# Performance work log

Measured on AMD Instinct MI355X. Metric: run time of the kernel, lower is better.

## Reference

```python
import jax, jax.numpy as jnp
import numpy as np

B, T, C = 2, 2048, 1024
H, DK, OUT = 16, 64, 1024


def setup_inputs() -> dict:
    key = jax.random.key(0)
    k1, k2, k3, k4, k5 = jax.random.split(key, 5)
    glorot_qkv = (2.0 / (C + H * DK)) ** 0.5  # glorot_normal stddev for [C,H,DK]
    glorot_o = (2.0 / (H * DK + OUT)) ** 0.5
    return {
        "x": jax.random.normal(k1, (B, T, C), dtype=jnp.float32),
        "query_mat": jax.random.normal(k2, (C, H, DK), dtype=jnp.float32) * glorot_qkv,
        "key_mat": jax.random.normal(k3, (C, H, DK), dtype=jnp.float32) * glorot_qkv,
        "value_mat": jax.random.normal(k4, (C, H, DK), dtype=jnp.float32) * glorot_qkv,
        "linear_m1": jax.random.normal(k5, (H * DK, OUT), dtype=jnp.float32) * glorot_o,
    }


def reference(x, query_mat, key_mat, value_mat, linear_m1):
    # x: [B,T,C]; projections: [C,H,DK]
    q = jnp.einsum('btc,chd->bhtd', x, query_mat)
    k = jnp.einsum('btc,chd->bhtd', x, key_mat)
    v = jnp.einsum('btc,chd->bhtd', x, value_mat)
    d_k = query_mat.shape[-1]
    # NOTE: faithful to source, which MULTIPLIES by sqrt(d_k)
    w = jnp.einsum('bhtd,bhzd->bhtz', q, k) * (d_k ** 0.5)
    t = w.shape[-1]
    causal = jnp.tril(jnp.ones((t, t), dtype=bool))  # [T,T]
    w = jnp.where(causal, w, -jnp.inf)
    w = jax.nn.softmax(w, axis=-1)
    # dropout inactive (training=False)
    o = jnp.einsum('bhtz,bhzd->bhtd', w, v)
    o = o.transpose(0, 2, 1, 3).reshape(o.shape[0], o.shape[2], -1)  # [B,T,H*DK]
    return jnp.einsum('btc,cz->btz', o, linear_m1)
```

## Files before the change

### kernel.cpp

```cpp
#include <hip/hip_runtime.h>


typedef unsigned short u16;
typedef unsigned int u32;
typedef unsigned long long u64;
typedef __attribute__((ext_vector_type(8))) short bf16x8;
typedef __attribute__((ext_vector_type(4))) float f32x4;

__device__ inline u16 f2bf(float f) {
  union { float f; unsigned u; } v; v.f = f;
  unsigned r = v.u + 0x7FFFu + ((v.u >> 16) & 1u);
  return (u16)(r >> 16);
}
__device__ inline float bf2f(u16 h) {
  union { unsigned u; float f; } v; v.u = ((unsigned)h) << 16;
  return v.f;
}
__device__ inline void glds16(const u16* g, u16* s) {
  __builtin_amdgcn_global_load_lds(
      (const __attribute__((address_space(1))) u32*)g,
      (__attribute__((address_space(3))) u32*)s, 16, 0, 0);
}
#define MFMA __builtin_amdgcn_mfma_f32_16x16x32_bf16

__global__ __launch_bounds__(256) void split_cast(const float* __restrict__ src,
                                                  u16* __restrict__ hi,
                                                  u16* __restrict__ lo, int n) {
  int i = (blockIdx.x * 256 + threadIdx.x) * 4;
  if (i >= n) return;
  float4 v = *(const float4*)(src + i);
  ushort4 h, l;
  h.x = f2bf(v.x); l.x = f2bf(v.x - bf2f(h.x));
  h.y = f2bf(v.y); l.y = f2bf(v.y - bf2f(h.y));
  h.z = f2bf(v.z); l.z = f2bf(v.z - bf2f(h.z));
  h.w = f2bf(v.w); l.w = f2bf(v.w - bf2f(h.w));
  *(ushort4*)(hi + i) = h;
  *(ushort4*)(lo + i) = l;
}

__global__ __launch_bounds__(256) void transpose_cast(const float* __restrict__ W,
                                                      u16* __restrict__ Wt) {
  __shared__ float tile[32][33];
  int bx = blockIdx.x * 32, by = blockIdx.y * 32;
  int tx = threadIdx.x, ty = threadIdx.y;
#pragma unroll
  for (int j = 0; j < 32; j += 8)
    tile[ty + j][tx] = W[(size_t)(by + ty + j) * 1024 + bx + tx];
  __syncthreads();
#pragma unroll
  for (int j = 0; j < 32; j += 8)
    Wt[(size_t)(bx + ty + j) * 1024 + by + tx] = f2bf(tile[tx][ty + j]);
}

__global__ __launch_bounds__(256) void transpose_cast_split(const float* __restrict__ W,
                                                            u16* __restrict__ Wth,
                                                            u16* __restrict__ Wtl) {
  __shared__ float tile[32][33];
  int bx = blockIdx.x * 32, by = blockIdx.y * 32;
  int tx = threadIdx.x, ty = threadIdx.y;
#pragma unroll
  for (int j = 0; j < 32; j += 8)
    tile[ty + j][tx] = W[(size_t)(by + ty + j) * 1024 + bx + tx];
  __syncthreads();
#pragma unroll
  for (int j = 0; j < 32; j += 8) {
    float v = tile[tx][ty + j];
    u16 h = f2bf(v);
    size_t idx = (size_t)(bx + ty + j) * 1024 + by + tx;
    Wth[idx] = h;
    Wtl[idx] = f2bf(v - bf2f(h));
  }
}

__global__ __launch_bounds__(256) void gemm_qkv(
    const u16* __restrict__ Xh, const u16* __restrict__ Xl,
    const u16* __restrict__ Wqh, const u16* __restrict__ Wql,
    const u16* __restrict__ Wkh, const u16* __restrict__ Wkl,
    const u16* __restrict__ Wvt,
    u16* __restrict__ Qh, u16* __restrict__ Ql,
    u16* __restrict__ Kh, u16* __restrict__ Kl,
    u16* __restrict__ Vt) {
  __shared__ u16 S[4][128][32];
  const int K = 1024;
  const int z = blockIdx.z;
  const bool split = (z < 2);
  const u16* Bh = (z == 0) ? Wqh : (z == 1) ? Wkh : Wvt;
  const u16* Bl = (z == 0) ? Wql : Wkl;
  const int tid = threadIdx.x;
  const int lane = tid & 63, wv = tid >> 6;
  const int quad = lane >> 4, lc = lane & 15;
  const int m0 = blockIdx.y * 128, n0 = blockIdx.x * 128;
  const int wm = (wv >> 1) * 64, wn = (wv & 1) * 64;
  const int lrow = lane >> 2, lk = (lane & 3) * 8;
  const u16* a0p = Xh + (size_t)(m0 + wv * 32 + lrow) * K + lk;
  const u16* a1p = a0p + 16 * K;
  const u16* al0p = Xl + (size_t)(m0 + wv * 32 + lrow) * K + lk;
  const u16* al1p = al0p + 16 * K;
  const u16* b0p = Bh + (size_t)(n0 + wv * 32 + lrow) * K + lk;
  const u16* b1p = b0p + 16 * K;
  const u16* bl0p = split ? (Bl + (size_t)(n0 + wv * 32 + lrow) * K + lk) : b0p;
  const u16* bl1p = bl0p + 16 * K;
  u16* sA0 = &S[0][wv * 32][0];      u16* sA1 = &S[0][wv * 32 + 16][0];
  u16* sAl0 = &S[1][wv * 32][0];     u16* sAl1 = &S[1][wv * 32 + 16][0];
  u16* sB0 = &S[2][wv * 32][0];      u16* sB1 = &S[2][wv * 32 + 16][0];
  u16* sBl0 = &S[3][wv * 32][0];     u16* sBl1 = &S[3][wv * 32 + 16][0];
  f32x4 acc[4][4];
#pragma unroll
  for (int i = 0; i < 4; i++)
#pragma unroll
    for (int j = 0; j < 4; j++) acc[i][j] = (f32x4){0.f, 0.f, 0.f, 0.f};
  for (int kc = 0; kc < K; kc += 32) {
    __syncthreads();
    glds16(a0p + kc, sA0); glds16(a1p + kc, sA1);
    glds16(b0p + kc, sB0); glds16(b1p + kc, sB1);
    if (split) {
      glds16(al0p + kc, sAl0); glds16(al1p + kc, sAl1);
      glds16(bl0p + kc, sBl0); glds16(bl1p + kc, sBl1);
    }
    __syncthreads();
    bf16x8 ah[4], al[4];
#pragma unroll
    for (int mt = 0; mt < 4; mt++)
      ah[mt] = *(const bf16x8*)&S[0][wm + mt * 16 + lc][quad * 8];
    if (split) {
#pragma unroll
      for (int mt = 0; mt < 4; mt++)
        al[mt] = *(const bf16x8*)&S[1][wm + mt * 16 + lc][quad * 8];
    }
#pragma unroll
    for (int nt = 0; nt < 4; nt++) {
      bf16x8 bfh = *(const bf16x8*)&S[2][wn + nt * 16 + lc][quad * 8];
#pragma unroll
      for (int mt = 0; mt < 4; mt++)
        acc[mt][nt] = MFMA(ah[mt], bfh, acc[mt][nt], 0, 0, 0);
      if (split) {
        bf16x8 bfl = *(const bf16x8*)&S[3][wn + nt * 16 + lc][quad * 8];
#pragma unroll
        for (int mt = 0; mt < 4; mt++) {
          acc[mt][nt] = MFMA(ah[mt], bfl, acc[mt][nt], 0, 0, 0);
          acc[mt][nt] = MFMA(al[mt], bfh, acc[mt][nt], 0, 0, 0);
        }
      }
    }
  }
  const int rb = quad * 4;
  if (z == 2) {
#pragma unroll
    for (int mt = 0; mt < 4; mt++)
#pragma unroll
      for (int nt = 0; nt < 4; nt++)
#pragma unroll
        for (int r = 0; r < 4; r++) {
          int m = m0 + wm + mt * 16 + rb + r, n = n0 + wn + nt * 16 + lc;
          int b = m >> 11, t = m & 2047, h = n >> 6, d = n & 63;
          Vt[((size_t)(b * 16 + h) * 64 + d) * 2048 + t] = f2bf(acc[mt][nt][r]);
        }
  } else {
    u16* Ch = (z == 0) ? Qh : Kh;
    u16* Cl = (z == 0) ? Ql : Kl;
    const float scale = (z == 0) ? 8.0f : 1.0f;
#pragma unroll
    for (int mt = 0; mt < 4; mt++)
#pragma unroll
      for (int nt = 0; nt < 4; nt++)
#pragma unroll
        for (int r = 0; r < 4; r++) {
          int m = m0 + wm + mt * 16 + rb + r, n = n0 + wn + nt * 16 + lc;
          int b = m >> 11, t = m & 2047, h = n >> 6, d = n & 63;
          float v = acc[mt][nt][r] * scale;
          u16 hv = f2bf(v);
          size_t idx = ((size_t)(b * 16 + h) * 2048 + t) * 64 + d;
          Ch[idx] = hv;
          Cl[idx] = f2bf(v - bf2f(hv));
        }
  }
}

__global__ __launch_bounds__(256) void gemm_out(const u16* __restrict__ A,
                                                const u16* __restrict__ Bt,
                                                float* __restrict__ C) {
  __shared__ u16 Sa[64][32], Sb[128][32];
  const int K = 1024, N = 1024;
  const int tid = threadIdx.x;
  const int lane = tid & 63, wv = tid >> 6;
  const int quad = lane >> 4, lc = lane & 15;
  const int m0 = blockIdx.y * 64, n0 = blockIdx.x * 128;
  const int wm = (wv >> 1) * 32, wn = (wv & 1) * 64;
  const int lrow = lane >> 2, lk = (lane & 3) * 8;
  const u16* ap = A + (size_t)(m0 + wv * 16 + lrow) * K + lk;
  const u16* b0p = Bt + (size_t)(n0 + wv * 32 + lrow) * K + lk;
  const u16* b1p = b0p + 16 * K;
  u16* sA = &Sa[wv * 16][0];
  u16* sB0 = &Sb[wv * 32][0];
  u16* sB1 = &Sb[wv * 32 + 16][0];
  f32x4 acc[2][4];
#pragma unroll
  for (int i = 0; i < 2; i++)
#pragma unroll
    for (int j = 0; j < 4; j++) acc[i][j] = (f32x4){0.f, 0.f, 0.f, 0.f};
  for (int kc = 0; kc < K; kc += 32) {
    __syncthreads();
    glds16(ap + kc, sA);
    glds16(b0p + kc, sB0);
    glds16(b1p + kc, sB1);
    __syncthreads();
    bf16x8 ah[2];
#pragma unroll
    for (int mt = 0; mt < 2; mt++)
      ah[mt] = *(const bf16x8*)&Sa[wm + mt * 16 + lc][quad * 8];
#pragma unroll
    for (int nt = 0; nt < 4; nt++) {
      bf16x8 bfh = *(const bf16x8*)&Sb[wn + nt * 16 + lc][quad * 8];
#pragma unroll
      for (int mt = 0; mt < 2; mt++)
        acc[mt][nt] = MFMA(ah[mt], bfh, acc[mt][nt], 0, 0, 0);
    }
  }
#pragma unroll
  for (int mt = 0; mt < 2; mt++)
#pragma unroll
    for (int nt = 0; nt < 4; nt++)
#pragma unroll
      for (int r = 0; r < 4; r++)
        C[(size_t)(m0 + wm + mt * 16 + quad * 4 + r) * N + n0 + wn + nt * 16 + lc] =
            acc[mt][nt][r];
}

__global__ __launch_bounds__(256, 4) void attn(const u16* __restrict__ Qh,
                                               const u16* __restrict__ Ql,
                                               const u16* __restrict__ Kh,
                                               const u16* __restrict__ Kl,
                                               const u16* __restrict__ Vt,
                                               u16* __restrict__ O16) {
  __shared__ u16 Khs[64][64], Kls[64][64], Vs[64][64];
  __shared__ u16 Ps[4][16][72];
  const int tid = threadIdx.x;
  const int lane = tid & 63, w = tid >> 6;
  const int quad = lane >> 4, lc = lane & 15;
  const int i = blockIdx.x;
  const int bh = i & 31;
  const int qb = 31 - (i >> 5);
  const int ng = qb + 1;
  const int tq = qb * 64 + w * 16 + lc;
  const size_t kbase = (size_t)bh * 2048 * 64;
  const size_t vbase = (size_t)bh * 64 * 2048;
  const size_t qoff = kbase + (size_t)tq * 64 + quad * 8;
  bf16x8 qh0 = *(const bf16x8*)(Qh + qoff);
  bf16x8 qh1 = *(const bf16x8*)(Qh + qoff + 32);
  bf16x8 ql0 = *(const bf16x8*)(Ql + qoff);
  bf16x8 ql1 = *(const bf16x8*)(Ql + qoff + 32);
  const int srow = lane >> 3;
  const int scol = (lane & 7) ^ srow;
  const u16* kg0 = Kh + kbase + (size_t)(w * 16 + srow) * 64 + scol * 8;
  const u16* kg1 = kg0 + 8 * 64;
  const u16* lg0 = Kl + kbase + (size_t)(w * 16 + srow) * 64 + scol * 8;
  const u16* lg1 = lg0 + 8 * 64;
  const u16* vg0 = Vt + vbase + (size_t)(w * 16 + srow) * 2048 + scol * 8;
  const u16* vg1 = vg0 + 8 * 2048;
  u16* kd0 = &Khs[w * 16][0];      u16* kd1 = &Khs[w * 16 + 8][0];
  u16* ld0 = &Kls[w * 16][0];      u16* ld1 = &Kls[w * 16 + 8][0];
  u16* vd0 = &Vs[w * 16][0];       u16* vd1 = &Vs[w * 16 + 8][0];

  float mi = -3.0e38f, li = 0.f;
  f32x4 o[4];
#pragma unroll
  for (int d = 0; d < 4; d++) o[d] = (f32x4){0.f, 0.f, 0.f, 0.f};
  const int rx = lc & 7;

  for (int g = 0; g < ng; g++) {
    const int z0 = g * 64;
    __syncthreads();
    glds16(kg0 + (size_t)z0 * 64, kd0); glds16(kg1 + (size_t)z0 * 64, kd1);
    glds16(lg0 + (size_t)z0 * 64, ld0); glds16(lg1 + (size_t)z0 * 64, ld1);
    glds16(vg0 + z0, vd0);              glds16(vg1 + z0, vd1);
    __syncthreads();
    f32x4 s[4];
#pragma unroll
    for (int tt = 0; tt < 4; tt++) {
      const int R = tt * 16 + lc;
      bf16x8 kh0 = *(const bf16x8*)&Khs[R][(quad ^ rx) * 8];
      bf16x8 kh1 = *(const bf16x8*)&Khs[R][((4 + quad) ^ rx) * 8];
      bf16x8 kl0 = *(const bf16x8*)&Kls[R][(quad ^ rx) * 8];
      bf16x8 kl1 = *(const bf16x8*)&Kls[R][((4 + quad) ^ rx) * 8];
      f32x4 sv = (f32x4){0.f, 0.f, 0.f, 0.f};
      sv = MFMA(kh0, qh0, sv, 0, 0, 0);
      sv = MFMA(kh1, qh1, sv, 0, 0, 0);
      sv = MFMA(kh0, ql0, sv, 0, 0, 0);
      sv = MFMA(kh1, ql1, sv, 0, 0, 0);
      sv = MFMA(kl0, qh0, sv, 0, 0, 0);
      sv = MFMA(kl1, qh1, sv, 0, 0, 0);
      s[tt] = sv;
    }
    if (g == ng - 1) {
#pragma unroll
      for (int tt = 0; tt < 4; tt++)
#pragma unroll
        for (int r = 0; r < 4; r++)
          if (z0 + tt * 16 + quad * 4 + r > tq) s[tt][r] = -3.0e38f;
    }
    float smax = -3.0e38f;
#pragma unroll
    for (int tt = 0; tt < 4; tt++)
#pragma unroll
      for (int r = 0; r < 4; r++) smax = fmaxf(smax, s[tt][r]);
    smax = fmaxf(smax, __shfl_xor(smax, 16));
    smax = fmaxf(smax, __shfl_xor(smax, 32));
    float mnew = fmaxf(mi, smax);
    float alpha = __expf(mi - mnew);
    mi = mnew;
    float rs = 0.f;
#pragma unroll
    for (int tt = 0; tt < 4; tt++) {
      union { u16 h[4]; u64 d; } pk;
#pragma unroll
      for (int r = 0; r < 4; r++) {
        float p = __expf(s[tt][r] - mnew);
        rs += p;
        pk.h[r] = f2bf(p);
      }
      *(u64*)&Ps[w][lc][tt * 16 + quad * 4] = pk.d;
    }
    li = li * alpha + rs;
#pragma unroll
    for (int d = 0; d < 4; d++) o[d] *= alpha;
    bf16x8 pf0 = *(const bf16x8*)&Ps[w][lc][quad * 8];
    bf16x8 pf1 = *(const bf16x8*)&Ps[w][lc][32 + quad * 8];
#pragma unroll
    for (int dd = 0; dd < 4; dd++) {
      const int R = dd * 16 + lc;
      bf16x8 va0 = *(const bf16x8*)&Vs[R][(quad ^ rx) * 8];
      bf16x8 va1 = *(const bf16x8*)&Vs[R][((4 + quad) ^ rx) * 8];
      o[dd] = MFMA(va0, pf0, o[dd], 0, 0, 0);
      o[dd] = MFMA(va1, pf1, o[dd], 0, 0, 0);
    }
  }
  li += __shfl_xor(li, 16);
  li += __shfl_xor(li, 32);
  const float rli = 1.0f / li;
  const int b = bh >> 4, hh = bh & 15;
  const size_t obase = ((size_t)(b * 2048 + tq)) * 1024 + hh * 64 + quad * 4;
#pragma unroll
  for (int dd = 0; dd < 4; dd++) {
    ushort4 ov;
    ov.x = f2bf(o[dd][0] * rli);
    ov.y = f2bf(o[dd][1] * rli);
    ov.z = f2bf(o[dd][2] * rli);
    ov.w = f2bf(o[dd][3] * rli);
    *(ushort4*)&O16[obase + dd * 16] = ov;
  }
}

extern "C" void kernel_launch(void* const* d_in, const int* in_sizes, int n_in,
                              void* d_out, int out_size, void* d_ws, size_t ws_size,
                              hipStream_t stream) {
  const float* x  = (const float*)d_in[0];
  const float* wq = (const float*)d_in[1];
  const float* wk = (const float*)d_in[2];
  const float* wv = (const float*)d_in[3];
  const float* wo = (const float*)d_in[4];

  char* w = (char*)d_ws;
  const size_t MB = 1u << 20;
  u16* Xh  = (u16*)(w + 0 * MB);
  u16* Xl  = (u16*)(w + 8 * MB);
  u16* Wqh = (u16*)(w + 16 * MB);
  u16* Wql = (u16*)(w + 18 * MB);
  u16* Wkh = (u16*)(w + 20 * MB);
  u16* Wkl = (u16*)(w + 22 * MB);
  u16* Wvt = (u16*)(w + 24 * MB);
  u16* Wot = (u16*)(w + 26 * MB);
  u16* Qhb = (u16*)(w + 28 * MB);
  u16* Qlb = (u16*)(w + 36 * MB);
  u16* Khb = (u16*)(w + 44 * MB);
  u16* Klb = (u16*)(w + 52 * MB);
  u16* Vtb = (u16*)(w + 60 * MB);
  u16* O16 = (u16*)(w + 0 * MB);

  hipLaunchKernelGGL(split_cast, dim3(4096), dim3(256), 0, stream, x, Xh, Xl, 4194304);
  dim3 tb(32, 8), tg(32, 32);
  hipLaunchKernelGGL(transpose_cast_split, tg, tb, 0, stream, wq, Wqh, Wql);
  hipLaunchKernelGGL(transpose_cast_split, tg, tb, 0, stream, wk, Wkh, Wkl);
  hipLaunchKernelGGL(transpose_cast, tg, tb, 0, stream, wv, Wvt);
  hipLaunchKernelGGL(transpose_cast, tg, tb, 0, stream, wo, Wot);

  hipLaunchKernelGGL(gemm_qkv, dim3(8, 32, 3), dim3(256), 0, stream,
                     Xh, Xl, Wqh, Wql, Wkh, Wkl, Wvt, Qhb, Qlb, Khb, Klb, Vtb);

  hipLaunchKernelGGL(attn, dim3(1024), dim3(256), 0, stream,
                     Qhb, Qlb, Khb, Klb, Vtb, O16);

  hipLaunchKernelGGL(gemm_out, dim3(8, 64), dim3(256), 0, stream, O16, Wot, (float*)d_out);
}
```

Baseline: 225.1 us.

## Double-buffer attention K/V tiles and fuse prep casts into one kernel

The attention kernel now double-buffers the Kh, Kl and V tiles in shared memory. The next tile's global_load_lds is issued before computing on the current tile, so load latency can overlap with the MFMA work, and one barrier per iteration is dropped. Launch bounds are relaxed from 4 to 2 waves per SIMD to give more registers alongside the doubled LDS footprint. The five preprocessing kernels (split cast of x, transpose-cast of the four weights) are merged into a single launch with blockIdx.z choosing the job, which removes launch overhead. The overlap depends on the compiler not inserting a full vmcnt wait before the LDS reads, which would serialise the prefetch again.

```diff
diff --git a/kernel.cpp b/kernel.cpp
--- a/kernel.cpp
+++ b/kernel.cpp
@@ -23,52 +23,56 @@
 }
 #define MFMA __builtin_amdgcn_mfma_f32_16x16x32_bf16
 
-__global__ __launch_bounds__(256) void split_cast(const float* __restrict__ src,
-                                                  u16* __restrict__ hi,
-                                                  u16* __restrict__ lo, int n) {
-  int i = (blockIdx.x * 256 + threadIdx.x) * 4;
-  if (i >= n) return;
-  float4 v = *(const float4*)(src + i);
-  ushort4 h, l;
-  h.x = f2bf(v.x); l.x = f2bf(v.x - bf2f(h.x));
-  h.y = f2bf(v.y); l.y = f2bf(v.y - bf2f(h.y));
-  h.z = f2bf(v.z); l.z = f2bf(v.z - bf2f(h.z));
-  h.w = f2bf(v.w); l.w = f2bf(v.w - bf2f(h.w));
-  *(ushort4*)(hi + i) = h;
-  *(ushort4*)(lo + i) = l;
-}
-
-__global__ __launch_bounds__(256) void transpose_cast(const float* __restrict__ W,
-                                                      u16* __restrict__ Wt) {
+__global__ __launch_bounds__(256) void prep(
+    const float* __restrict__ x,
+    const float* __restrict__ wq, const float* __restrict__ wk,
+    const float* __restrict__ wv, const float* __restrict__ wo,
+    u16* __restrict__ Xh, u16* __restrict__ Xl,
+    u16* __restrict__ Wqh, u16* __restrict__ Wql,
+    u16* __restrict__ Wkh, u16* __restrict__ Wkl,
+    u16* __restrict__ Wvt, u16* __restrict__ Wot) {
+  const int z = blockIdx.z;
+  const int tid = threadIdx.x;
+  if (z == 0) {
+    const int bid = blockIdx.y * 32 + blockIdx.x;
+#pragma unroll
+    for (int k = 0; k < 4; k++) {
+      int i = bid * 4096 + k * 1024 + tid * 4;
+      float4 v = *(const float4*)(x + i);
+      ushort4 h, l;
+      h.x = f2bf(v.x); l.x = f2bf(v.x - bf2f(h.x));
+      h.y = f2bf(v.y); l.y = f2bf(v.y - bf2f(h.y));
+      h.z = f2bf(v.z); l.z = f2bf(v.z - bf2f(h.z));
+      h.w = f2bf(v.w); l.w = f2bf(v.w - bf2f(h.w));
+      *(ushort4*)(Xh + i) = h;
+      *(ushort4*)(Xl + i) = l;
+    }
+    return;
+  }
   __shared__ float tile[32][33];
-  int bx = blockIdx.x * 32, by = blockIdx.y * 32;
-  int tx = threadIdx.x, ty = threadIdx.y;
+  const float* W = (z == 1) ? wq : (z == 2) ? wk : (z == 3) ? wv : wo;
+  const int bx = blockIdx.x * 32, by = blockIdx.y * 32;
+  const int tx = tid & 31, ty = tid >> 5;
 #pragma unroll
   for (int j = 0; j < 32; j += 8)
     tile[ty + j][tx] = W[(size_t)(by + ty + j) * 1024 + bx + tx];
   __syncthreads();
-#pragma unroll
-  for (int j = 0; j < 32; j += 8)
-    Wt[(size_t)(bx + ty + j) * 1024 + by + tx] = f2bf(tile[tx][ty + j]);
-}
-
-__global__ __launch_bounds__(256) void transpose_cast_split(const float* __restrict__ W,
-                                                            u16* __restrict__ Wth,
-                                                            u16* __restrict__ Wtl) {
-  __shared__ float tile[32][33];
-  int bx = blockIdx.x * 32, by = blockIdx.y * 32;
-  int tx = threadIdx.x, ty = threadIdx.y;
-#pragma unroll
-  for (int j = 0; j < 32; j += 8)
-    tile[ty + j][tx] = W[(size_t)(by + ty + j) * 1024 + bx + tx];
-  __syncthreads();
-#pragma unroll
-  for (int j = 0; j < 32; j += 8) {
-    float v = tile[tx][ty + j];
-    u16 h = f2bf(v);
-    size_t idx = (size_t)(bx + ty + j) * 1024 + by + tx;
-    Wth[idx] = h;
-    Wtl[idx] = f2bf(v - bf2f(h));
+  if (z <= 2) {
+    u16* Th = (z == 1) ? Wqh : Wkh;
+    u16* Tl = (z == 1) ? Wql : Wkl;
+#pragma unroll
+    for (int j = 0; j < 32; j += 8) {
+      float v = tile[tx][ty + j];
+      u16 h = f2bf(v);
+      size_t idx = (size_t)(bx + ty + j) * 1024 + by + tx;
+      Th[idx] = h;
+      Tl[idx] = f2bf(v - bf2f(h));
+    }
+  } else {
+    u16* T = (z == 3) ? Wvt : Wot;
+#pragma unroll
+    for (int j = 0; j < 32; j += 8)
+      T[(size_t)(bx + ty + j) * 1024 + by + tx] = f2bf(tile[tx][ty + j]);
   }
 }
 
@@ -226,13 +230,13 @@
             acc[mt][nt][r];
 }
 
-__global__ __launch_bounds__(256, 4) void attn(const u16* __restrict__ Qh,
+__global__ __launch_bounds__(256, 2) void attn(const u16* __restrict__ Qh,
                                                const u16* __restrict__ Ql,
                                                const u16* __restrict__ Kh,
                                                const u16* __restrict__ Kl,
                                                const u16* __restrict__ Vt,
                                                u16* __restrict__ O16) {
-  __shared__ u16 Khs[64][64], Kls[64][64], Vs[64][64];
+  __shared__ u16 Khs[2][64][64], Kls[2][64][64], Vs[2][64][64];
   __shared__ u16 Ps[4][16][72];
   const int tid = threadIdx.x;
   const int lane = tid & 63, w = tid >> 6;
@@ -252,14 +256,8 @@
   const int srow = lane >> 3;
   const int scol = (lane & 7) ^ srow;
   const u16* kg0 = Kh + kbase + (size_t)(w * 16 + srow) * 64 + scol * 8;
-  const u16* kg1 = kg0 + 8 * 64;
   const u16* lg0 = Kl + kbase + (size_t)(w * 16 + srow) * 64 + scol * 8;
-  const u16* lg1 = lg0 + 8 * 64;
   const u16* vg0 = Vt + vbase + (size_t)(w * 16 + srow) * 2048 + scol * 8;
-  const u16* vg1 = vg0 + 8 * 2048;
-  u16* kd0 = &Khs[w * 16][0];      u16* kd1 = &Khs[w * 16 + 8][0];
-  u16* ld0 = &Kls[w * 16][0];      u16* ld1 = &Kls[w * 16 + 8][0];
-  u16* vd0 = &Vs[w * 16][0];       u16* vd1 = &Vs[w * 16 + 8][0];
 
   float mi = -3.0e38f, li = 0.f;
   f32x4 o[4];
@@ -267,21 +265,33 @@
   for (int d = 0; d < 4; d++) o[d] = (f32x4){0.f, 0.f, 0.f, 0.f};
   const int rx = lc & 7;
 
+  {
+    glds16(kg0, &Khs[0][w * 16][0]); glds16(kg0 + 8 * 64, &Khs[0][w * 16 + 8][0]);
+    glds16(lg0, &Kls[0][w * 16][0]); glds16(lg0 + 8 * 64, &Kls[0][w * 16 + 8][0]);
+    glds16(vg0, &Vs[0][w * 16][0]);  glds16(vg0 + 8 * 2048, &Vs[0][w * 16 + 8][0]);
+  }
   for (int g = 0; g < ng; g++) {
+    const int buf = g & 1;
     const int z0 = g * 64;
     __syncthreads();
-    glds16(kg0 + (size_t)z0 * 64, kd0); glds16(kg1 + (size_t)z0 * 64, kd1);
-    glds16(lg0 + (size_t)z0 * 64, ld0); glds16(lg1 + (size_t)z0 * 64, ld1);
-    glds16(vg0 + z0, vd0);              glds16(vg1 + z0, vd1);
-    __syncthreads();
+    if (g + 1 < ng) {
+      const int zn = (g + 1) * 64;
+      const int nb = buf ^ 1;
+      glds16(kg0 + (size_t)zn * 64, &Khs[nb][w * 16][0]);
+      glds16(kg0 + (size_t)zn * 64 + 8 * 64, &Khs[nb][w * 16 + 8][0]);
+      glds16(lg0 + (size_t)zn * 64, &Kls[nb][w * 16][0]);
+      glds16(lg0 + (size_t)zn * 64 + 8 * 64, &Kls[nb][w * 16 + 8][0]);
+      glds16(vg0 + zn, &Vs[nb][w * 16][0]);
+      glds16(vg0 + zn + 8 * 2048, &Vs[nb][w * 16 + 8][0]);
+    }
     f32x4 s[4];
 #pragma unroll
     for (int tt = 0; tt < 4; tt++) {
       const int R = tt * 16 + lc;
-      bf16x8 kh0 = *(const bf16x8*)&Khs[R][(quad ^ rx) * 8];
-      bf16x8 kh1 = *(const bf16x8*)&Khs[R][((4 + quad) ^ rx) * 8];
-      bf16x8 kl0 = *(const bf16x8*)&Kls[R][(quad ^ rx) * 8];
-      bf16x8 kl1 = *(const bf16x8*)&Kls[R][((4 + quad) ^ rx) * 8];
+      bf16x8 kh0 = *(const bf16x8*)&Khs[buf][R][(quad ^ rx) * 8];
+      bf16x8 kh1 = *(const bf16x8*)&Khs[buf][R][((4 + quad) ^ rx) * 8];
+      bf16x8 kl0 = *(const bf16x8*)&Kls[buf][R][(quad ^ rx) * 8];
+      bf16x8 kl1 = *(const bf16x8*)&Kls[buf][R][((4 + quad) ^ rx) * 8];
       f32x4 sv = (f32x4){0.f, 0.f, 0.f, 0.f};
       sv = MFMA(kh0, qh0, sv, 0, 0, 0);
       sv = MFMA(kh1, qh1, sv, 0, 0, 0);
@@ -328,8 +338,8 @@
 #pragma unroll
     for (int dd = 0; dd < 4; dd++) {
       const int R = dd * 16 + lc;
-      bf16x8 va0 = *(const bf16x8*)&Vs[R][(quad ^ rx) * 8];
-      bf16x8 va1 = *(const bf16x8*)&Vs[R][((4 + quad) ^ rx) * 8];
+      bf16x8 va0 = *(const bf16x8*)&Vs[buf][R][(quad ^ rx) * 8];
+      bf16x8 va1 = *(const bf16x8*)&Vs[buf][R][((4 + quad) ^ rx) * 8];
       o[dd] = MFMA(va0, pf0, o[dd], 0, 0, 0);
       o[dd] = MFMA(va1, pf1, o[dd], 0, 0, 0);
     }
@@ -376,12 +386,8 @@
   u16* Vtb = (u16*)(w + 60 * MB);
   u16* O16 = (u16*)(w + 0 * MB);
 
-  hipLaunchKernelGGL(split_cast, dim3(4096), dim3(256), 0, stream, x, Xh, Xl, 4194304);
-  dim3 tb(32, 8), tg(32, 32);
-  hipLaunchKernelGGL(transpose_cast_split, tg, tb, 0, stream, wq, Wqh, Wql);
-  hipLaunchKernelGGL(transpose_cast_split, tg, tb, 0, stream, wk, Wkh, Wkl);
-  hipLaunchKernelGGL(transpose_cast, tg, tb, 0, stream, wv, Wvt);
-  hipLaunchKernelGGL(transpose_cast, tg, tb, 0, stream, wo, Wot);
+  hipLaunchKernelGGL(prep, dim3(32, 32, 5), dim3(256), 0, stream,
+                     x, wq, wk, wv, wo, Xh, Xl, Wqh, Wql, Wkh, Wkl, Wvt, Wot);
 
   hipLaunchKernelGGL(gemm_qkv, dim3(8, 32, 3), dim3(256), 0, stream,
                      Xh, Xl, Wqh, Wql, Wkh, Wkl, Wvt, Qhb, Qlb, Khb, Klb, Vtb);
```

Result: faster. 214.3 us (-4.8%).
